# Kernel tuning notes

Hardware: AMD Instinct MI355X
Metric: run time of the kernel (lower is better)

The kernel has to match this reference:

```python
import jax, jax.numpy as jnp
import numpy as np

NUM_GROUPS = 4
KERNEL_SIZE = 3


def _conv1x1(x, w, b):
    # x: [B,Cin,H,W], w: [Cout,Cin], b: [Cout]
    return jnp.einsum('bchw,oc->bohw', x, w) + b[None, :, None, None]


def _unfold(t, ks):
    # t: [B,G,Gd,H,W] -> patches [B,G,Gd,ks*ks,H,W] with zero padding (pad=ks//2)
    pad = ks // 2
    H, W = t.shape[-2:]
    tp = jnp.pad(t, ((0, 0), (0, 0), (0, 0), (pad, pad), (pad, pad)))
    return jnp.stack([tp[..., i:i + H, j:j + W]
                      for i in range(ks) for j in range(ks)], axis=3)


def setup_inputs() -> dict:
    key = jax.random.key(0)
    ks = jax.random.split(key, 7)
    B, Cin, C, H, W = 4, 256, 256, 64, 64
    s = 1.0 / np.sqrt(Cin)
    return {
        'x': jax.random.normal(ks[0], (B, Cin, H, W), dtype=jnp.float32),
        'wq': jax.random.normal(ks[1], (C, Cin), dtype=jnp.float32) * s,
        'bq': jax.random.normal(ks[2], (C,), dtype=jnp.float32) * 0.01,
        'wk': jax.random.normal(ks[3], (C, Cin), dtype=jnp.float32) * s,
        'bk': jax.random.normal(ks[4], (C,), dtype=jnp.float32) * 0.01,
        'wv': jax.random.normal(ks[5], (C, Cin), dtype=jnp.float32) * s,
        'bv': jax.random.normal(ks[6], (C,), dtype=jnp.float32) * 0.01,
    }


def reference(x, wq, bq, wk, bk, wv, bv):
    B, _, H, W = x.shape
    C = wq.shape[0]
    G = NUM_GROUPS
    Gd = C // G
    q = _conv1x1(x, wq, bq).reshape(B, G, Gd, H, W)
    k = _conv1x1(x, wk, bk).reshape(B, G, Gd, H, W)
    v = _conv1x1(x, wv, bv).reshape(B, G, Gd, H, W)
    kp = _unfold(k, KERNEL_SIZE)  # [B,G,Gd,k2,H,W]
    vp = _unfold(v, KERNEL_SIZE)  # [B,G,Gd,k2,H,W]
    attn = jnp.einsum('bgdhw,bgdphw->bgphw', q, kp)  # [B,G,k2,H,W]
    attn = jax.nn.softmax(attn, axis=2)
    out = jnp.einsum('bgphw,bgdphw->bgdhw', attn, vp)  # [B,G,Gd,H,W]
    return out.reshape(B, C, H, W)
```

## Files before the change

kernel.cpp:

```cpp
#include <hip/hip_runtime.h>
#include <cstddef>
#include <cstdint>

#define BDIM 4
#define HH   64
#define WW   64
#define NG   4
#define GD   64
#define HWSZ 4096
#define NTOT 16384
#define CIN  256

typedef __attribute__((ext_vector_type(4))) float f32x4;
typedef _Float16 f16x4_t __attribute__((ext_vector_type(4)));
typedef _Float16 f16x8_t __attribute__((ext_vector_type(8)));

__device__ __forceinline__ void lds_load16(const void* g, void* l) {
    __builtin_amdgcn_global_load_lds(
        (const __attribute__((address_space(1))) unsigned int*)g,
        (__attribute__((address_space(3))) unsigned int*)l, 16, 0, 0);
}

__global__ __launch_bounds__(256, 3) void qkv_gemm_kernel(
    const float* __restrict__ x,
    const float* __restrict__ wq, const float* __restrict__ bq,
    const float* __restrict__ wk, const float* __restrict__ bk,
    const float* __restrict__ wv, const float* __restrict__ bv,
    _Float16* __restrict__ qh, _Float16* __restrict__ kh,
    _Float16* __restrict__ vh)
{
    __shared__ float    As[2][128 * 32];
    __shared__ _Float16 Bs[2][128 * 32];

    const int t  = threadIdx.x;
    const int bx = blockIdx.x;
    const int u  = (bx & 7) * 96 + (bx >> 3);
    const int mt = u % 6;
    const int nt = u / 6;

    const int l     = t & 63;
    const int wid   = t >> 6;
    const int wm    = wid >> 1, wn = wid & 1;
    const int lrow  = l & 15;
    const int grp   = l >> 4;
    const int lrow4 = grp * 4;

    const float* wsel = (mt < 2) ? wq : (mt < 4) ? wk : wv;
    const float* bsel = (mt < 2) ? bq : (mt < 4) ? bk : bv;
    _Float16*    osel = (mt < 2) ? qh : (mt < 4) ? kh : vh;
    const int    mtl  = mt & 1;

    const int bi  = nt >> 5;
    const int px0 = (nt & 31) * 128;

    f32x4 acc[4][4];
    #pragma unroll
    for (int mi = 0; mi < 4; ++mi) {
        const f32x4 bb = *(const f32x4*)&bsel[mtl * 128 + wm * 64 + mi * 16 + lrow4];
        #pragma unroll
        for (int ni = 0; ni < 4; ++ni) acc[mi][ni] = bb;
    }

    const float* asrc[4];
    #pragma unroll
    for (int i = 0; i < 4; ++i) {
        const int w16 = i * 256 + t;
        const int m  = w16 >> 3;
        const int kb = w16 & 7;
        asrc[i] = wsel + (size_t)(mtl * 128 + m) * CIN + ((kb ^ (m & 7)) * 4);
    }

    const int spx  = t & 127;
    const int sko0 = t >> 7;
    const float* xbp = x + (size_t)bi * CIN * HWSZ + px0 + spx;
    const int bw0 = spx * 32 + ((sko0       ^ (spx & 3)) * 8);
    const int bw1 = spx * 32 + (((sko0 + 2) ^ (spx & 3)) * 8);

    {
        #pragma unroll
        for (int i = 0; i < 4; ++i)
            lds_load16(asrc[i], &As[0][(i * 256 + t) * 4]);
        float r0[8], r1[8];
        #pragma unroll
        for (int j = 0; j < 8; ++j) r0[j] = xbp[(size_t)(sko0 * 8 + j) * HWSZ];
        #pragma unroll
        for (int j = 0; j < 8; ++j) r1[j] = xbp[(size_t)((sko0 + 2) * 8 + j) * HWSZ];
        f16x8_t w0, w1;
        #pragma unroll
        for (int j = 0; j < 8; ++j) { w0[j] = (_Float16)r0[j]; w1[j] = (_Float16)r1[j]; }
        *(f16x8_t*)&Bs[0][bw0] = w0;
        *(f16x8_t*)&Bs[0][bw1] = w1;
        __syncthreads();
    }

    for (int kt = 0; kt < 8; ++kt) {
        const int cur = kt & 1, nxt = cur ^ 1;

        float r0[8], r1[8];
        if (kt < 7) {
            const int kb = (kt + 1) * 32;
            #pragma unroll
            for (int i = 0; i < 4; ++i)
                lds_load16(asrc[i] + kb, &As[nxt][(i * 256 + t) * 4]);
            #pragma unroll
            for (int j = 0; j < 8; ++j) r0[j] = xbp[(size_t)(kb + sko0 * 8 + j) * HWSZ];
            #pragma unroll
            for (int j = 0; j < 8; ++j) r1[j] = xbp[(size_t)(kb + (sko0 + 2) * 8 + j) * HWSZ];
        }

        f16x8_t af[4];
        #pragma unroll
        for (int mi = 0; mi < 4; ++mi) {
            const int m = wm * 64 + mi * 16 + lrow;
            const int s = m & 7;
            const f32x4 a0 = *(const f32x4*)&As[cur][m * 32 + ((2 * grp) ^ s) * 4];
            const f32x4 a1 = *(const f32x4*)&As[cur][m * 32 + ((2 * grp + 1) ^ s) * 4];
            f16x8_t f;
            #pragma unroll
            for (int j = 0; j < 4; ++j) { f[j] = (_Float16)a0[j]; f[4 + j] = (_Float16)a1[j]; }
            af[mi] = f;
        }
        f16x8_t bf[4];
        #pragma unroll
        for (int ni = 0; ni < 4; ++ni) {
            const int px = wn * 64 + ni * 16 + lrow;
            bf[ni] = *(const f16x8_t*)&Bs[cur][px * 32 + ((grp ^ (px & 3)) * 8)];
        }
        #pragma unroll
        for (int mi = 0; mi < 4; ++mi)
            #pragma unroll
            for (int ni = 0; ni < 4; ++ni)
                acc[mi][ni] = __builtin_amdgcn_mfma_f32_16x16x32_f16(
                    af[mi], bf[ni], acc[mi][ni], 0, 0, 0);

        if (kt < 7) {
            f16x8_t w0, w1;
            #pragma unroll
            for (int j = 0; j < 8; ++j) { w0[j] = (_Float16)r0[j]; w1[j] = (_Float16)r1[j]; }
            *(f16x8_t*)&Bs[nxt][bw0] = w0;
            *(f16x8_t*)&Bs[nxt][bw1] = w1;
        }
        __syncthreads();
    }

    #pragma unroll
    for (int ni = 0; ni < 4; ++ni) {
        const size_t ng = (size_t)(nt * 128 + wn * 64 + ni * 16 + lrow);
        #pragma unroll
        for (int mi = 0; mi < 4; ++mi) {
            f16x4_t hv;
            #pragma unroll
            for (int j = 0; j < 4; ++j) hv[j] = (_Float16)acc[mi][ni][j];
            const int chunk = mtl * 8 + wm * 4 + mi;
            *(f16x4_t*)&osel[((size_t)chunk * NTOT + ng) * 16 + lrow4] = hv;
        }
    }
}

__global__ __launch_bounds__(256) void loc_attn_kernel(
    const _Float16* __restrict__ qh, const _Float16* __restrict__ kh,
    const _Float16* __restrict__ vh, float* __restrict__ out)
{
    const int t   = threadIdx.x;
    const int bx0 = blockIdx.x;
    const int bx  = (bx0 & 7) * 128 + (bx0 >> 3);
    const int h = bx & 63;
    const int g = (bx >> 6) & 3;
    const int b = bx >> 8;

    const int wl  = t & 15;
    const int c   = (t >> 4) & 3;
    const int wid = t >> 6;
    const int w   = wid * 16 + wl;

    const int ck = g * 4 + c;
    const size_t n = (size_t)b * HWSZ + h * 64 + w;

    float qf[16];
    {
        const _Float16* qp = &qh[((size_t)ck * NTOT + n) * 16];
        const f16x8_t q0 = *(const f16x8_t*)qp;
        const f16x8_t q1 = *(const f16x8_t*)(qp + 8);
        #pragma unroll
        for (int j = 0; j < 8; ++j) { qf[j] = (float)q0[j]; qf[8 + j] = (float)q1[j]; }
    }

    float logit[9];
    #pragma unroll
    for (int p = 0; p < 9; ++p) {
        const int dh = p / 3 - 1, dw = p % 3 - 1;
        const int hh = h + dh, ww2 = w + dw;
        float part = 0.f;
        if (hh >= 0 && hh < HH && ww2 >= 0 && ww2 < WW) {
            const size_t nn = (size_t)b * HWSZ + hh * 64 + ww2;
            const _Float16* kp = &kh[((size_t)ck * NTOT + nn) * 16];
            const f16x8_t k0 = *(const f16x8_t*)kp;
            const f16x8_t k1 = *(const f16x8_t*)(kp + 8);
            #pragma unroll
            for (int j = 0; j < 8; ++j)
                part += qf[j] * (float)k0[j] + qf[8 + j] * (float)k1[j];
        }
        part += __shfl_xor(part, 16, 64);
        part += __shfl_xor(part, 32, 64);
        logit[p] = part;
    }

    float mx = logit[0];
    #pragma unroll
    for (int p = 1; p < 9; ++p) mx = fmaxf(mx, logit[p]);
    float a[9];
    float s = 0.f;
    #pragma unroll
    for (int p = 0; p < 9; ++p) { a[p] = __expf(logit[p] - mx); s += a[p]; }
    const float inv = 1.f / s;
    #pragma unroll
    for (int p = 0; p < 9; ++p) a[p] *= inv;

    float acc[16];
    #pragma unroll
    for (int dd = 0; dd < 16; ++dd) acc[dd] = 0.f;
    #pragma unroll
    for (int p = 0; p < 9; ++p) {
        const int dh = p / 3 - 1, dw = p % 3 - 1;
        const int hh = h + dh, ww2 = w + dw;
        if (hh < 0 || hh >= HH || ww2 < 0 || ww2 >= WW) continue;
        const size_t nn = (size_t)b * HWSZ + hh * 64 + ww2;
        const _Float16* vp = &vh[((size_t)ck * NTOT + nn) * 16];
        const f16x8_t v0 = *(const f16x8_t*)vp;
        const f16x8_t v1 = *(const f16x8_t*)(vp + 8);
        const float ap = a[p];
        #pragma unroll
        for (int j = 0; j < 8; ++j) {
            acc[j]     += ap * (float)v0[j];
            acc[8 + j] += ap * (float)v1[j];
        }
    }

    const int obase = b * 256 + g * 64 + c * 16;
    const int off = h * 64 + w;
    #pragma unroll
    for (int dd = 0; dd < 16; ++dd)
        out[(size_t)(obase + dd) * HWSZ + off] = acc[dd];
}

extern "C" void kernel_launch(void* const* d_in, const int* in_sizes, int n_in,
                              void* d_out, int out_size, void* d_ws, size_t ws_size,
                              hipStream_t stream) {
    const float* x  = (const float*)d_in[0];
    const float* wq = (const float*)d_in[1];
    const float* bq = (const float*)d_in[2];
    const float* wk = (const float*)d_in[3];
    const float* bk = (const float*)d_in[4];
    const float* wv = (const float*)d_in[5];
    const float* bv = (const float*)d_in[6];
    float* out = (float*)d_out;

    char* ws = (char*)d_ws;
    _Float16* qh = (_Float16*)ws;
    _Float16* kh = (_Float16*)(ws + 8388608);
    _Float16* vh = (_Float16*)(ws + 16777216);

    qkv_gemm_kernel<<<dim3(768), 256, 0, stream>>>(x, wq, bq, wk, bk, wv, bv,
                                                   qh, kh, vh);
    loc_attn_kernel<<<dim3(1024), 256, 0, stream>>>(qh, kh, vh, out);
}
```

Baseline: 33.71 us.

## Stage weight tile as fp16 in LDS in two halves instead of fp32 double-buffer

The A-operand (weight) staging changes from fp32 async global-to-LDS double-buffered 32-wide k-slices to a single 128x128 fp16 LDS tile loaded twice (k 0-127, then 128-255). Weights are converted to fp16 once at staging, with a 16-way XOR swizzle. The goal is to remove the per-iteration fp32-to-fp16 conversion of A fragments and halve A's LDS read traffic. The cost is synchronous register-staged weight loads with a stall at the halfway point, since the second half is loaded without overlap between two barriers. The k loop is also fully unrolled.

```diff
diff --git a/kernel.cpp b/kernel.cpp
--- a/kernel.cpp
+++ b/kernel.cpp
@@ -15,12 +15,6 @@
 typedef _Float16 f16x4_t __attribute__((ext_vector_type(4)));
 typedef _Float16 f16x8_t __attribute__((ext_vector_type(8)));
 
-__device__ __forceinline__ void lds_load16(const void* g, void* l) {
-    __builtin_amdgcn_global_load_lds(
-        (const __attribute__((address_space(1))) unsigned int*)g,
-        (__attribute__((address_space(3))) unsigned int*)l, 16, 0, 0);
-}
-
 __global__ __launch_bounds__(256, 3) void qkv_gemm_kernel(
     const float* __restrict__ x,
     const float* __restrict__ wq, const float* __restrict__ bq,
@@ -29,7 +23,7 @@
     _Float16* __restrict__ qh, _Float16* __restrict__ kh,
     _Float16* __restrict__ vh)
 {
-    __shared__ float    As[2][128 * 32];
+    __shared__ _Float16 Ap[128 * 128];
     __shared__ _Float16 Bs[2][128 * 32];
 
     const int t  = threadIdx.x;
@@ -61,14 +55,10 @@
         for (int ni = 0; ni < 4; ++ni) acc[mi][ni] = bb;
     }
 
-    const float* asrc[4];
-    #pragma unroll
-    for (int i = 0; i < 4; ++i) {
-        const int w16 = i * 256 + t;
-        const int m  = w16 >> 3;
-        const int kb = w16 & 7;
-        asrc[i] = wsel + (size_t)(mtl * 128 + m) * CIN + ((kb ^ (m & 7)) * 4);
-    }
+    const int smA = t >> 1;
+    const int khA = (t & 1) * 64;
+    const float* wrow = wsel + (size_t)(mtl * 128 + smA) * CIN + khA;
+    const int aswz = smA & 15;
 
     const int spx  = t & 127;
     const int sko0 = t >> 7;
@@ -76,10 +66,25 @@
     const int bw0 = spx * 32 + ((sko0       ^ (spx & 3)) * 8);
     const int bw1 = spx * 32 + (((sko0 + 2) ^ (spx & 3)) * 8);
 
+    #pragma unroll
+    for (int c = 0; c < 4; ++c) {
+        float fl[16];
+        #pragma unroll
+        for (int q4 = 0; q4 < 4; ++q4) {
+            const float4 v = *(const float4*)(wrow + c * 16 + q4 * 4);
+            fl[q4 * 4 + 0] = v.x; fl[q4 * 4 + 1] = v.y;
+            fl[q4 * 4 + 2] = v.z; fl[q4 * 4 + 3] = v.w;
+        }
+        #pragma unroll
+        for (int hs = 0; hs < 2; ++hs) {
+            const int slot = (khA >> 3) + c * 2 + hs;
+            f16x8_t w8;
+            #pragma unroll
+            for (int j = 0; j < 8; ++j) w8[j] = (_Float16)fl[hs * 8 + j];
+            *(f16x8_t*)&Ap[smA * 128 + ((slot ^ aswz) << 3)] = w8;
+        }
+    }
     {
-        #pragma unroll
-        for (int i = 0; i < 4; ++i)
-            lds_load16(asrc[i], &As[0][(i * 256 + t) * 4]);
         float r0[8], r1[8];
         #pragma unroll
         for (int j = 0; j < 8; ++j) r0[j] = xbp[(size_t)(sko0 * 8 + j) * HWSZ];
@@ -90,37 +95,29 @@
         for (int j = 0; j < 8; ++j) { w0[j] = (_Float16)r0[j]; w1[j] = (_Float16)r1[j]; }
         *(f16x8_t*)&Bs[0][bw0] = w0;
         *(f16x8_t*)&Bs[0][bw1] = w1;
-        __syncthreads();
-    }
-
-    for (int kt = 0; kt < 8; ++kt) {
-        const int cur = kt & 1, nxt = cur ^ 1;
+    }
+    __syncthreads();
+
+    #pragma unroll
+    for (int s = 0; s < 8; ++s) {
+        const int cur = s & 1, nxt = cur ^ 1;
+        const int kt  = s & 3;
 
         float r0[8], r1[8];
-        if (kt < 7) {
-            const int kb = (kt + 1) * 32;
-            #pragma unroll
-            for (int i = 0; i < 4; ++i)
-                lds_load16(asrc[i] + kb, &As[nxt][(i * 256 + t) * 4]);
+        if (s < 7) {
+            const int kb = (s + 1) * 32;
             #pragma unroll
             for (int j = 0; j < 8; ++j) r0[j] = xbp[(size_t)(kb + sko0 * 8 + j) * HWSZ];
             #pragma unroll
             for (int j = 0; j < 8; ++j) r1[j] = xbp[(size_t)(kb + (sko0 + 2) * 8 + j) * HWSZ];
         }
 
-        f16x8_t af[4];
+        f16x8_t af[4], bf[4];
         #pragma unroll
         for (int mi = 0; mi < 4; ++mi) {
             const int m = wm * 64 + mi * 16 + lrow;
-            const int s = m & 7;
-            const f32x4 a0 = *(const f32x4*)&As[cur][m * 32 + ((2 * grp) ^ s) * 4];
-            const f32x4 a1 = *(const f32x4*)&As[cur][m * 32 + ((2 * grp + 1) ^ s) * 4];
-            f16x8_t f;
-            #pragma unroll
-            for (int j = 0; j < 4; ++j) { f[j] = (_Float16)a0[j]; f[4 + j] = (_Float16)a1[j]; }
-            af[mi] = f;
-        }
-        f16x8_t bf[4];
+            af[mi] = *(const f16x8_t*)&Ap[m * 128 + (((kt * 4 + grp) ^ (m & 15)) << 3)];
+        }
         #pragma unroll
         for (int ni = 0; ni < 4; ++ni) {
             const int px = wn * 64 + ni * 16 + lrow;
@@ -133,12 +130,34 @@
                 acc[mi][ni] = __builtin_amdgcn_mfma_f32_16x16x32_f16(
                     af[mi], bf[ni], acc[mi][ni], 0, 0, 0);
 
-        if (kt < 7) {
+        if (s < 7) {
             f16x8_t w0, w1;
             #pragma unroll
             for (int j = 0; j < 8; ++j) { w0[j] = (_Float16)r0[j]; w1[j] = (_Float16)r1[j]; }
             *(f16x8_t*)&Bs[nxt][bw0] = w0;
             *(f16x8_t*)&Bs[nxt][bw1] = w1;
+        }
+
+        if (s == 3) {
+            __syncthreads();
+            #pragma unroll
+            for (int c = 0; c < 4; ++c) {
+                float fl[16];
+                #pragma unroll
+                for (int q4 = 0; q4 < 4; ++q4) {
+                    const float4 v = *(const float4*)(wrow + 128 + c * 16 + q4 * 4);
+                    fl[q4 * 4 + 0] = v.x; fl[q4 * 4 + 1] = v.y;
+                    fl[q4 * 4 + 2] = v.z; fl[q4 * 4 + 3] = v.w;
+                }
+                #pragma unroll
+                for (int hs = 0; hs < 2; ++hs) {
+                    const int slot = (khA >> 3) + c * 2 + hs;
+                    f16x8_t w8;
+                    #pragma unroll
+                    for (int j = 0; j < 8; ++j) w8[j] = (_Float16)fl[hs * 8 + j];
+                    *(f16x8_t*)&Ap[smA * 128 + ((slot ^ aswz) << 3)] = w8;
+                }
+            }
         }
         __syncthreads();
     }
```

Result: slower. 41.19 us (+22.2%).
